# Performance work log

Measured on AMD Instinct MI355X. Metric: run time of the kernel, lower is better.

The kernel has to match this reference:

```python
import jax, jax.numpy as jnp
import numpy as np
from math import factorial, sqrt

LMAX = 5
TAUS = [16, 16, 16, 16, 16, 16]
BATCH = 256


def _cg(j1, m1, j2, m2, j, m):
    """Standard (complex SO(3) basis) Clebsch-Gordan coefficient <j1 m1 j2 m2 | j m>."""
    if m1 + m2 != m or j < abs(j1 - j2) or j > j1 + j2:
        return 0.0
    f = factorial
    pref = sqrt((2 * j + 1) * f(j + j1 - j2) * f(j - j1 + j2) * f(j1 + j2 - j) / f(j1 + j2 + j + 1))
    pref *= sqrt(f(j + m) * f(j - m) * f(j1 - m1) * f(j1 + m1) * f(j2 - m2) * f(j2 + m2))
    kmin = max(0, j2 - j - m1, j1 + m2 - j)
    kmax = min(j1 + j2 - j, j1 - m1, j2 + m2)
    s = 0.0
    for k in range(kmin, kmax + 1):
        s += (-1) ** k / (f(k) * f(j1 + j2 - j - k) * f(j1 - m1 - k) * f(j2 + m2 - k)
                          * f(j - j2 + m1 + k) * f(j - j1 - m2 + k))
    return pref * s


def _pairs():
    # default CGNet ltuples: for each output l, all (l1, l2) with l1 <= l2 and triangle ineq.
    out = []
    for l in range(LMAX + 1):
        for l1 in range(LMAX + 1):
            for l2 in range(l1, LMAX + 1):
                if abs(l1 - l2) <= l <= l1 + l2:
                    out.append((l, l1, l2))
    return out


PAIRS = _pairs()  # 69 (l, l1, l2) tuples for lmax=5


def _cg_mat(l, l1, l2):
    M = np.zeros((2 * l1 + 1, 2 * l2 + 1, 2 * l + 1), dtype=np.float32)
    for m1 in range(-l1, l1 + 1):
        for m2 in range(-l2, l2 + 1):
            m = m1 + m2
            if -l <= m <= l:
                M[m1 + l1, m2 + l2, m + l] = _cg(l1, m1, l2, m2, l, m)
    return M


CG_MATS = {p: _cg_mat(*p) for p in PAIRS}
CUM_TAUS = np.concatenate([[0], (np.asarray(TAUS) * (2 * np.arange(LMAX + 1) + 1)).cumsum()]).astype(int)


def setup_inputs() -> dict:
    key = jax.random.key(0)
    Fs = jax.random.normal(key, (BATCH, int(CUM_TAUS[-1]), 2), dtype=jnp.float32)
    return {"Fs": Fs}


def reference(Fs) -> jnp.ndarray:
    """Sparse CG tensor product: for each (l,l1,l2) combine fragments F_l1, F_l2
    with CG coefficients into the l-output fragment; concat all fragments.
    Output: (B, cumu_tm_FF[-1], 2) with (m, tau) flattening per l fragment."""
    B = Fs.shape[0]
    frR, frI = [], []
    for l in range(LMAX + 1):
        seg = Fs[:, CUM_TAUS[l]:CUM_TAUS[l + 1]].reshape(B, 2 * l + 1, TAUS[l], 2)
        frR.append(seg[..., 0])
        frI.append(seg[..., 1])
    outs = [[] for _ in range(LMAX + 1)]
    for (l, l1, l2) in PAIRS:
        cg = jnp.asarray(CG_MATS[(l, l1, l2)])  # (2l1+1, 2l2+1, 2l+1)
        r1, i1, r2, i2 = frR[l1], frI[l1], frR[l2], frI[l2]
        e = lambda a, b: jnp.einsum('xym,bxi,byj->bmij', cg, a, b)
        oR = e(r1, r2) - e(i1, i2)           # complex multiply, real part
        oI = e(r1, i2) + e(i1, r2)           # imag part
        # (B, 2l+1, tau1*tau2, 2)
        outs[l].append(jnp.stack([oR, oI], axis=-1).reshape(B, 2 * l + 1, -1, 2))
    # per-l: concat channel blocks (t_offsets order), flatten (m, tau), concat over l
    return jnp.concatenate(
        [jnp.concatenate(outs[l], axis=2).reshape(B, -1, 2) for l in range(LMAX + 1)], axis=1)
```

## Files before the change

### kernel.cpp

```cpp
#include <hip/hip_runtime.h>
#include <vector>
#include <cmath>
#include <cstdint>


#define LMAXV 5
#define NTAU 16

static const int CUMT[7] = {0, 16, 64, 144, 256, 400, 576};
__host__ __device__ constexpr int cumt_ce(int l) {
    int s = 0; for (int a = 0; a < l; ++a) s += 16 * (2 * a + 1); return s;
}

constexpr int F_ROWS   = 576;
constexpr int NBATCH   = 256;
constexpr int F4_PER_B = 457 * 128;
constexpr int BLK      = 256;
constexpr int NCHUNK   = 8;
constexpr int NJOBS    = 457;
constexpr int NCOEF    = 2211;
constexpr int MAXJC    = 58;

typedef float f32x4 __attribute__((ext_vector_type(4)));


static double factd(int n) { double r = 1.0; for (int i = 2; i <= n; ++i) r *= (double)i; return r; }

static double cg_coef(int j1, int m1, int j2, int m2, int j, int m) {
    if (m1 + m2 != m) return 0.0;
    double pref = std::sqrt((2.0 * j + 1.0) * factd(j + j1 - j2) * factd(j - j1 + j2) *
                            factd(j1 + j2 - j) / factd(j1 + j2 + j + 1));
    pref *= std::sqrt(factd(j + m) * factd(j - m) * factd(j1 - m1) * factd(j1 + m1) *
                      factd(j2 - m2) * factd(j2 + m2));
    int kmin = std::max(0, std::max(j2 - j - m1, j1 + m2 - j));
    int kmax = std::min(j1 + j2 - j, std::min(j1 - m1, j2 + m2));
    double s = 0.0;
    for (int k = kmin; k <= kmax; ++k) {
        s += ((k & 1) ? -1.0 : 1.0) /
             (factd(k) * factd(j1 + j2 - j - k) * factd(j1 - m1 - k) * factd(j2 + m2 - k) *
              factd(j - j2 + m1 + k) * factd(j - j1 - m2 + k));
    }
    return pref * s;
}

struct Tables { std::vector<int4> jobs; std::vector<float> coeffs; };

static const Tables& get_tables() {
    static Tables t = []() {
        Tables t;
        for (int l = 0; l <= LMAXV; ++l) {
            for (int m_idx = 0; m_idx < 2 * l + 1; ++m_idx) {
                int m = m_idx - l;
                for (int l1 = 0; l1 <= LMAXV; ++l1) {
                    for (int l2 = l1; l2 <= LMAXV; ++l2) {
                        if (!(std::abs(l1 - l2) <= l && l <= l1 + l2)) continue;
                        int lo = std::max(-l1, m - l2), hi = std::min(l1, m + l2);
                        int4 jb;
                        jb.x = (CUMT[l1] + lo + l1) | ((2 * l1 + 1) << 16);
                        jb.y = (CUMT[l2] / 2 + m - lo + l2) | ((2 * l2 + 1) << 16);
                        jb.z = hi - lo + 1;
                        jb.w = (int)t.coeffs.size();
                        for (int m1 = lo; m1 <= hi; ++m1)
                            t.coeffs.push_back((float)cg_coef(l1, m1, l2, m - m1, l, m));
                        t.jobs.push_back(jb);
                    }
                }
            }
        }
        return t;
    }();
    return t;
}


#define KBODY(N)                                                              \
    {                                                                         \
        float2 a[N]; f32x4 v[N]; float cc[N];                                 \
        _Pragma("unroll")                                                     \
        for (int k = 0; k < N; ++k) {                                         \
            a[k]  = pa[k];                                                    \
            v[k]  = pv[-k];                                                   \
            cc[k] = sC[coff + k];                                             \
        }                                                                     \
        _Pragma("unroll")                                                     \
        for (int k = 0; k < N; ++k) {                                         \
            aR0 = fmaf(cc[k], a[k].x * v[k].x - a[k].y * v[k].y, aR0);        \
            aI0 = fmaf(cc[k], a[k].x * v[k].y + a[k].y * v[k].x, aI0);        \
            aR1 = fmaf(cc[k], a[k].x * v[k].z - a[k].y * v[k].w, aR1);        \
            aI1 = fmaf(cc[k], a[k].x * v[k].w + a[k].y * v[k].z, aI1);        \
        }                                                                     \
    }

__global__ __launch_bounds__(256) void cg_tp_kernel(
    const float2* __restrict__ Fs, f32x4* __restrict__ out,
    const int4* __restrict__ jobs, const float* __restrict__ coeffs)
{
    __shared__ float2 sF1[F_ROWS];
    __shared__ f32x4  sF2[F_ROWS / 2];
    __shared__ float  sC[NCOEF];
    __shared__ int4   sJ[MAXJC];

    const int tid   = threadIdx.x;
    const int batch = blockIdx.x >> 3;
    const int chunk = blockIdx.x & (NCHUNK - 1);
    const int jbase = chunk * 57;
    const int jcnt  = (chunk == NCHUNK - 1) ? 58 : 57;

    const float2* __restrict__ Fb = Fs + (size_t)batch * F_ROWS;

#define STAGE_L(L)                                                            \
    {                                                                         \
        constexpr int base = cumt_ce(L);                                      \
        constexpr int w    = 2 * (L) + 1;                                     \
        for (int t = tid; t < 16 * w; t += BLK) {                             \
            int i = t / w, x = t - i * w;                                     \
            sF1[base + t] = Fb[base + x * 16 + i];                            \
        }                                                                     \
        for (int t = tid; t < 8 * w; t += BLK) {                              \
            int jp = t / w, y = t - jp * w;                                   \
            sF2[base / 2 + t] = *(const f32x4*)&Fb[base + y * 16 + 2 * jp];   \
        }                                                                     \
    }
    STAGE_L(0) STAGE_L(1) STAGE_L(2) STAGE_L(3) STAGE_L(4) STAGE_L(5)
#undef STAGE_L
    for (int t = tid; t < NCOEF; t += BLK) sC[t] = coeffs[t];
    for (int t = tid; t < jcnt;  t += BLK) sJ[t] = jobs[jbase + t];
    __syncthreads();

    const int half = tid >> 7;
    const int t128 = tid & 127;
    const int i    = t128 >> 3;
    const int jp   = t128 & 7;

    f32x4* __restrict__ outb = out + (size_t)batch * F4_PER_B + (size_t)jbase * 128 + t128;

    for (int jj = half; jj < jcnt; jj += 2) {
        const int4 jbv = sJ[jj];
        const int ax   = __builtin_amdgcn_readfirstlane(jbv.x);
        const int by   = __builtin_amdgcn_readfirstlane(jbv.y);
        const int cnt  = __builtin_amdgcn_readfirstlane(jbv.z);
        const int coff = __builtin_amdgcn_readfirstlane(jbv.w);

        const float2* __restrict__ pa = sF1 + (ax & 0xffff) + i  * (ax >> 16);
        const f32x4*  __restrict__ pv = sF2 + (by & 0xffff) + jp * (by >> 16);

        float aR0 = 0.f, aI0 = 0.f, aR1 = 0.f, aI1 = 0.f;
        switch (cnt) {
            case 1:  KBODY(1)  break;
            case 2:  KBODY(2)  break;
            case 3:  KBODY(3)  break;
            case 4:  KBODY(4)  break;
            case 5:  KBODY(5)  break;
            case 6:  KBODY(6)  break;
            case 7:  KBODY(7)  break;
            case 8:  KBODY(8)  break;
            case 9:  KBODY(9)  break;
            case 10: KBODY(10) break;
            default: KBODY(11) break;
        }

        f32x4 val; val.x = aR0; val.y = aI0; val.z = aR1; val.w = aI1;
        outb[(size_t)jj * 128] = val;
    }
}


extern "C" void kernel_launch(void* const* d_in, const int* in_sizes, int n_in,
                              void* d_out, int out_size, void* d_ws, size_t ws_size,
                              hipStream_t stream) {
    const Tables& t = get_tables();

    char*  ws       = (char*)d_ws;
    int4*  d_jobs   = (int4*)ws;
    size_t jbytes   = t.jobs.size() * sizeof(int4);
    size_t coff     = (jbytes + 255) & ~(size_t)255;
    float* d_coeffs = (float*)(ws + coff);

    hipMemcpyAsync(d_jobs, t.jobs.data(), jbytes, hipMemcpyHostToDevice, stream);
    hipMemcpyAsync(d_coeffs, t.coeffs.data(), t.coeffs.size() * sizeof(float),
                   hipMemcpyHostToDevice, stream);

    const float2* Fs  = (const float2*)d_in[0];
    f32x4*        out = (f32x4*)d_out;

    cg_tp_kernel<<<NBATCH * NCHUNK, BLK, 0, stream>>>(Fs, out, d_jobs, d_coeffs);
}
```

Measured before the change: 64.86 us.

## Compute 2x2 output micro-tiles per thread from a single unpermuted shared copy

```diff
diff --git a/kernel.cpp b/kernel.cpp
--- a/kernel.cpp
+++ b/kernel.cpp
@@ -8,16 +8,13 @@
 #define NTAU 16
 
 static const int CUMT[7] = {0, 16, 64, 144, 256, 400, 576};
-__host__ __device__ constexpr int cumt_ce(int l) {
-    int s = 0; for (int a = 0; a < l; ++a) s += 16 * (2 * a + 1); return s;
-}
 
 constexpr int F_ROWS   = 576;
+constexpr int F4_ROWS  = 288;
 constexpr int NBATCH   = 256;
 constexpr int F4_PER_B = 457 * 128;
 constexpr int BLK      = 256;
 constexpr int NCHUNK   = 8;
-constexpr int NJOBS    = 457;
 constexpr int NCOEF    = 2211;
 constexpr int MAXJC    = 58;
 
@@ -56,8 +53,8 @@
                         if (!(std::abs(l1 - l2) <= l && l <= l1 + l2)) continue;
                         int lo = std::max(-l1, m - l2), hi = std::min(l1, m + l2);
                         int4 jb;
-                        jb.x = (CUMT[l1] + lo + l1) | ((2 * l1 + 1) << 16);
-                        jb.y = (CUMT[l2] / 2 + m - lo + l2) | ((2 * l2 + 1) << 16);
+                        jb.x = (CUMT[l1] / 2 + (lo + l1) * 8) * 16;
+                        jb.y = (CUMT[l2] / 2 + (m - lo + l2) * 8) * 16;
                         jb.z = hi - lo + 1;
                         jb.w = (int)t.coeffs.size();
                         for (int m1 = lo; m1 <= hi; ++m1)
@@ -75,30 +72,33 @@
 
 #define KBODY(N)                                                              \
     {                                                                         \
-        float2 a[N]; f32x4 v[N]; float cc[N];                                 \
+        f32x4 a[N], v[N]; float cc[N];                                        \
         _Pragma("unroll")                                                     \
         for (int k = 0; k < N; ++k) {                                         \
-            a[k]  = pa[k];                                                    \
-            v[k]  = pv[-k];                                                   \
+            a[k]  = *(const f32x4*)(sFb + ax + k * 128);                      \
+            v[k]  = *(const f32x4*)(sFb + vy - k * 128);                      \
             cc[k] = sC[coff + k];                                             \
         }                                                                     \
         _Pragma("unroll")                                                     \
         for (int k = 0; k < N; ++k) {                                         \
-            aR0 = fmaf(cc[k], a[k].x * v[k].x - a[k].y * v[k].y, aR0);        \
-            aI0 = fmaf(cc[k], a[k].x * v[k].y + a[k].y * v[k].x, aI0);        \
-            aR1 = fmaf(cc[k], a[k].x * v[k].z - a[k].y * v[k].w, aR1);        \
-            aI1 = fmaf(cc[k], a[k].x * v[k].w + a[k].y * v[k].z, aI1);        \
+            r00 = fmaf(cc[k], a[k].x * v[k].x - a[k].y * v[k].y, r00);        \
+            i00 = fmaf(cc[k], a[k].x * v[k].y + a[k].y * v[k].x, i00);        \
+            r01 = fmaf(cc[k], a[k].x * v[k].z - a[k].y * v[k].w, r01);        \
+            i01 = fmaf(cc[k], a[k].x * v[k].w + a[k].y * v[k].z, i01);        \
+            r10 = fmaf(cc[k], a[k].z * v[k].x - a[k].w * v[k].y, r10);        \
+            i10 = fmaf(cc[k], a[k].z * v[k].y + a[k].w * v[k].x, i10);        \
+            r11 = fmaf(cc[k], a[k].z * v[k].z - a[k].w * v[k].w, r11);        \
+            i11 = fmaf(cc[k], a[k].z * v[k].w + a[k].w * v[k].z, i11);        \
         }                                                                     \
     }
 
 __global__ __launch_bounds__(256) void cg_tp_kernel(
-    const float2* __restrict__ Fs, f32x4* __restrict__ out,
+    const f32x4* __restrict__ Fs, f32x4* __restrict__ out,
     const int4* __restrict__ jobs, const float* __restrict__ coeffs)
 {
-    __shared__ float2 sF1[F_ROWS];
-    __shared__ f32x4  sF2[F_ROWS / 2];
-    __shared__ float  sC[NCOEF];
-    __shared__ int4   sJ[MAXJC];
+    __shared__ f32x4 sF[F4_ROWS];
+    __shared__ float sC[NCOEF];
+    __shared__ int4  sJ[MAXJC];
 
     const int tid   = threadIdx.x;
     const int batch = blockIdx.x >> 3;
@@ -106,45 +106,33 @@
     const int jbase = chunk * 57;
     const int jcnt  = (chunk == NCHUNK - 1) ? 58 : 57;
 
-    const float2* __restrict__ Fb = Fs + (size_t)batch * F_ROWS;
-
-#define STAGE_L(L)                                                            \
-    {                                                                         \
-        constexpr int base = cumt_ce(L);                                      \
-        constexpr int w    = 2 * (L) + 1;                                     \
-        for (int t = tid; t < 16 * w; t += BLK) {                             \
-            int i = t / w, x = t - i * w;                                     \
-            sF1[base + t] = Fb[base + x * 16 + i];                            \
-        }                                                                     \
-        for (int t = tid; t < 8 * w; t += BLK) {                              \
-            int jp = t / w, y = t - jp * w;                                   \
-            sF2[base / 2 + t] = *(const f32x4*)&Fb[base + y * 16 + 2 * jp];   \
-        }                                                                     \
+    {
+        const f32x4* __restrict__ Fb4 = Fs + (size_t)batch * F4_ROWS;
+        for (int t = tid; t < F4_ROWS; t += BLK) sF[t] = Fb4[t];
+        for (int t = tid; t < NCOEF;   t += BLK) sC[t] = coeffs[t];
+        for (int t = tid; t < jcnt;    t += BLK) sJ[t] = jobs[jbase + t];
     }
-    STAGE_L(0) STAGE_L(1) STAGE_L(2) STAGE_L(3) STAGE_L(4) STAGE_L(5)
-#undef STAGE_L
-    for (int t = tid; t < NCOEF; t += BLK) sC[t] = coeffs[t];
-    for (int t = tid; t < jcnt;  t += BLK) sJ[t] = jobs[jbase + t];
     __syncthreads();
 
-    const int half = tid >> 7;
-    const int t128 = tid & 127;
-    const int i    = t128 >> 3;
-    const int jp   = t128 & 7;
+    const int wv   = tid >> 6;
+    const int lane = tid & 63;
+    const int ip   = lane >> 3;
+    const int jp   = lane & 7;
+    const char* __restrict__ sFb = (const char*)sF;
 
-    f32x4* __restrict__ outb = out + (size_t)batch * F4_PER_B + (size_t)jbase * 128 + t128;
+    f32x4* __restrict__ outb =
+        out + (size_t)batch * F4_PER_B + (size_t)jbase * 128;
 
-    for (int jj = half; jj < jcnt; jj += 2) {
+    for (int jj = wv; jj < jcnt; jj += 4) {
         const int4 jbv = sJ[jj];
-        const int ax   = __builtin_amdgcn_readfirstlane(jbv.x);
-        const int by   = __builtin_amdgcn_readfirstlane(jbv.y);
+        const int ax   = __builtin_amdgcn_readfirstlane(jbv.x) + ip * 16;
+        const int vy   = __builtin_amdgcn_readfirstlane(jbv.y) + jp * 16;
         const int cnt  = __builtin_amdgcn_readfirstlane(jbv.z);
         const int coff = __builtin_amdgcn_readfirstlane(jbv.w);
 
-        const float2* __restrict__ pa = sF1 + (ax & 0xffff) + i  * (ax >> 16);
-        const f32x4*  __restrict__ pv = sF2 + (by & 0xffff) + jp * (by >> 16);
+        float r00 = 0.f, i00 = 0.f, r01 = 0.f, i01 = 0.f;
+        float r10 = 0.f, i10 = 0.f, r11 = 0.f, i11 = 0.f;
 
-        float aR0 = 0.f, aI0 = 0.f, aR1 = 0.f, aI1 = 0.f;
         switch (cnt) {
             case 1:  KBODY(1)  break;
             case 2:  KBODY(2)  break;
@@ -159,8 +147,11 @@
             default: KBODY(11) break;
         }
 
-        f32x4 val; val.x = aR0; val.y = aI0; val.z = aR1; val.w = aI1;
-        outb[(size_t)jj * 128] = val;
+        f32x4 s0; s0.x = r00; s0.y = i00; s0.z = r01; s0.w = i01;
+        f32x4 s1; s1.x = r10; s1.y = i10; s1.z = r11; s1.w = i11;
+        f32x4* __restrict__ po = outb + (size_t)jj * 128 + ip * 16 + jp;
+        po[0] = s0;
+        po[8] = s1;
     }
 }
 
@@ -180,8 +171,8 @@
     hipMemcpyAsync(d_coeffs, t.coeffs.data(), t.coeffs.size() * sizeof(float),
                    hipMemcpyHostToDevice, stream);
 
-    const float2* Fs  = (const float2*)d_in[0];
-    f32x4*        out = (f32x4*)d_out;
+    const f32x4* Fs  = (const f32x4*)d_in[0];
+    f32x4*       out = (f32x4*)d_out;
 
     cg_tp_kernel<<<NBATCH * NCHUNK, BLK, 0, stream>>>(Fs, out, d_jobs, d_coeffs);
 }
```

After: 57.57 us. 11.2% less time.
